# Kernel tuning notes

Measured on AMD Instinct MI355X. Metric: run time of the kernel, lower is better.

## Reference

```python
import jax, jax.numpy as jnp
import numpy as np
import math

D_MODEL = 128
N_HEAD = 8
D_K = D_MODEL // N_HEAD
NEG_INF = -1e30


def setup_inputs() -> dict:
    key = jax.random.key(0)
    ks = jax.random.split(key, 8)
    B, N, D = 4, 2048, D_MODEL
    s = 1.0 / math.sqrt(D)
    x = jax.random.normal(ks[0], (B, D, N), dtype=jnp.float32)
    mask = jnp.ones((B, N), dtype=jnp.float32)
    Wq = jax.random.normal(ks[1], (D, D), dtype=jnp.float32) * s
    Wk = jax.random.normal(ks[2], (D, D), dtype=jnp.float32) * s
    Wv = jax.random.normal(ks[3], (D, D), dtype=jnp.float32) * s
    Wfc = jax.random.normal(ks[4], (D, D), dtype=jnp.float32) * s
    z = jnp.zeros((D,), dtype=jnp.float32)
    return {"x": x, "mask": mask, "Wq": Wq, "bq": z, "Wk": Wk, "bk": z,
            "Wv": Wv, "bv": z, "Wfc": Wfc, "bfc": z}


def reference(x, mask, Wq, bq, Wk, bk, Wv, bv, Wfc, bfc):
    # x: [B, D, N], mask: [B, N]
    B, D, N = x.shape
    xt = jnp.swapaxes(x, 1, 2)  # [B, N, D]
    q = (xt @ Wq.T + bq).reshape(B, N, N_HEAD, D_K)
    k = (xt @ Wk.T + bk).reshape(B, N, N_HEAD, D_K)
    v = (xt @ Wv.T + bv).reshape(B, N, N_HEAD, D_K)
    # scores: [B, H, Nq, Nk]; NOTE: original scales by sqrt(d_model), not sqrt(d_k)
    scores = jnp.einsum('bnhd,bmhd->bhnm', q, k) / jnp.sqrt(jnp.float32(D))
    # multiplicative mask_logits over the key dimension
    m = mask[:, None, None, :]  # [B, 1, 1, Nk]
    scores = scores * m + (1.0 - m) * NEG_INF
    atten = jax.nn.softmax(scores, axis=-1)  # dropout is identity (p=0 / eval)
    out = jnp.einsum('bhnm,bmhd->bnhd', atten, v).reshape(B, N, D)
    out = out @ Wfc.T + bfc
    return jnp.swapaxes(out, 1, 2)  # [B, D, N]
```

## Files before the change

kernel.cpp:

```cpp
#include <hip/hip_runtime.h>
#include <stdint.h>

#define BSZ  4
#define NSEQ 2048
#define DM   128
#define NH   8
#define DK   16
#define LOG2E 1.4426950408889634f
#define SCALE_QL 0.1275156338341935f
#define M_FIX 18.0f

typedef __bf16          bf16x8v __attribute__((ext_vector_type(8)));
typedef float           f32x4   __attribute__((ext_vector_type(4)));
typedef float           f32x16  __attribute__((ext_vector_type(16)));
typedef unsigned short  u16x8   __attribute__((ext_vector_type(8)));
typedef unsigned short  u16x4   __attribute__((ext_vector_type(4)));
typedef unsigned int    u32x2   __attribute__((ext_vector_type(2)));
typedef unsigned int    u32x4   __attribute__((ext_vector_type(4)));

__device__ __forceinline__ unsigned short f2bf(float f) {
    unsigned u = __float_as_uint(f);
    u = (u + 0x7fffu + ((u >> 16) & 1u)) >> 16;
    return (unsigned short)u;
}

__device__ __forceinline__ unsigned int pack2bf(float a, float b) {
#if __has_builtin(__builtin_amdgcn_cvt_pk_bf16_f32)
    typedef __bf16 bf16x2 __attribute__((ext_vector_type(2)));
    bf16x2 v = __builtin_amdgcn_cvt_pk_bf16_f32(a, b);
    return __builtin_bit_cast(unsigned int, v);
#else
    return (unsigned)f2bf(a) | ((unsigned)f2bf(b) << 16);
#endif
}

__device__ __forceinline__ float exp2_(float x) {
#if __has_builtin(__builtin_amdgcn_exp2f)
    return __builtin_amdgcn_exp2f(x);
#else
    return exp2f(x);
#endif
}

__device__ __forceinline__ u16x8 cvt8(const float* p, float sc) {
    const f32x4 a = *reinterpret_cast<const f32x4*>(p);
    const f32x4 b = *reinterpret_cast<const f32x4*>(p + 4);
    u32x4 u = {pack2bf(a[0] * sc, a[1] * sc), pack2bf(a[2] * sc, a[3] * sc),
               pack2bf(b[0] * sc, b[1] * sc), pack2bf(b[2] * sc, b[3] * sc)};
    return __builtin_bit_cast(u16x8, u);
}

__device__ __forceinline__ f32x4 mfma16(u16x8 a, u16x8 b, f32x4 c) {
    return __builtin_amdgcn_mfma_f32_16x16x32_bf16(
        __builtin_bit_cast(bf16x8v, a), __builtin_bit_cast(bf16x8v, b), c, 0, 0, 0);
}
__device__ __forceinline__ f32x16 mfma32(u16x8 a, u16x8 b, f32x16 c) {
    return __builtin_amdgcn_mfma_f32_32x32x16_bf16(
        __builtin_bit_cast(bf16x8v, a), __builtin_bit_cast(bf16x8v, b), c, 0, 0, 0);
}

__global__ __launch_bounds__(192) void k_qkv(
    const float* __restrict__ x,
    const float* __restrict__ Wq, const float* __restrict__ bq,
    const float* __restrict__ Wk, const float* __restrict__ bk,
    const float* __restrict__ Wv, const float* __restrict__ bv,
    const float* __restrict__ Wfc, const float* __restrict__ mask,
    unsigned short* __restrict__ Q, unsigned short* __restrict__ Kb,
    unsigned short* __restrict__ Vt,
    unsigned short* __restrict__ WfcB, float* __restrict__ mbias)
{
    const int gt = blockIdx.x * 192 + threadIdx.x;
    if (gt < DM * DM) {
        WfcB[gt] = f2bf(Wfc[gt]);
    } else if (gt < DM * DM + BSZ * NSEQ) {
        const int i = gt - DM * DM;
        mbias[i] = (1.0f - mask[i]) * (-1e30f * LOG2E) - M_FIX;
    }

    const int lane = threadIdx.x & 63;
    const int mat  = threadIdx.x >> 6;
    const int c    = lane & 15;
    const int quad = lane >> 4;
    const int b    = blockIdx.x >> 8;
    const int n0   = ((blockIdx.x >> 1) & 127) << 4;
    const int th   = blockIdx.x & 1;

    u16x8 xf[4];
#pragma unroll
    for (int kk = 0; kk < 4; ++kk) {
        u16x8 u;
#pragma unroll
        for (int j = 0; j < 8; ++j)
            u[j] = f2bf(x[(b * DM + kk * 32 + quad * 8 + j) * NSEQ + n0 + c]);
        xf[kk] = u;
    }

    const float* W    = (mat == 0) ? Wq : (mat == 1) ? Wk : Wv;
    const float* bias = (mat == 0) ? bq : (mat == 1) ? bk : bv;
    const float  sc   = (mat == 0) ? SCALE_QL : 1.0f;

#pragma unroll
    for (int tt = 0; tt < 4; ++tt) {
        const int t = th * 4 + tt;
        f32x4 acc = {0.f, 0.f, 0.f, 0.f};
#pragma unroll
        for (int kk = 0; kk < 4; ++kk)
            acc = mfma16(cvt8(W + (t * 16 + c) * DM + kk * 32 + quad * 8, sc),
                         xf[kk], acc);
        if (mat == 2) {
#pragma unroll
            for (int r = 0; r < 4; ++r)
                Vt[((b * NH + t) * DK + quad * 4 + r) * NSEQ + n0 + c] =
                    f2bf(acc[r] + bias[t * 16 + quad * 4 + r]);
        } else {
            u16x4 pk;
#pragma unroll
            for (int r = 0; r < 4; ++r)
                pk[r] = f2bf(acc[r] + bias[t * 16 + quad * 4 + r] * sc);
            *reinterpret_cast<u16x4*>(
                (mat == 0 ? Q : Kb) + ((size_t)(b * NH + t) * NSEQ + n0 + c) * DK +
                quad * 4) = pk;
        }
    }
}

__global__ __launch_bounds__(256, 4) void k_attn(
    const unsigned short* __restrict__ Q,
    const unsigned short* __restrict__ Kb,
    const unsigned short* __restrict__ Vt,
    const float* __restrict__ mb2,
    unsigned short* __restrict__ AO)
{
    __shared__ __align__(16) char smem[17408];
    const int tid  = threadIdx.x;
    const int lane = tid & 63;
    const int w    = tid >> 6;
    const int q32  = lane & 31;
    const int hi   = lane >> 5;
    const int c    = lane & 15;
    const int quad = lane >> 4;

    const int b  = blockIdx.x >> 9;
    const int h  = (blockIdx.x >> 6) & 7;
    const int n0 = (blockIdx.x & 63) << 5;
    const int bh = b * NH + h;

    const u16x8 uq = *reinterpret_cast<const u16x8*>(
        Q + ((size_t)bh * NSEQ + n0 + q32) * DK + 8 * hi);

    const unsigned short* Kp = Kb + (size_t)bh * NSEQ * DK + 8 * hi;
    const unsigned short* Vp = Vt + ((size_t)bh * DK + c) * NSEQ + 8 * quad;
    const float*          mb = mb2 + b * NSEQ + 4 * hi;

    char* pbase = smem + w * 4352;
    char* wrow  = pbase + q32 * 136 + 8 * hi;
    const char* rrow0 = pbase + c * 136 + 16 * quad;
    const char* rrow1 = pbase + (c + 16) * 136 + 16 * quad;

    float l_acc = 0.f;
    f32x4 o0 = {0.f, 0.f, 0.f, 0.f}, o1 = {0.f, 0.f, 0.f, 0.f};
    const int kvb = w * (NSEQ / 4);

    for (int it = 0; it < 8; ++it) {
        const int kv0 = kvb + it * 64;
        f32x16 C0, C1;
#pragma unroll
        for (int g = 0; g < 4; ++g) {
            const f32x4 bg0 = *reinterpret_cast<const f32x4*>(mb + kv0 + 8 * g);
            const f32x4 bg1 = *reinterpret_cast<const f32x4*>(mb + kv0 + 32 + 8 * g);
#pragma unroll
            for (int r = 0; r < 4; ++r) {
                C0[4 * g + r] = bg0[r];
                C1[4 * g + r] = bg1[r];
            }
        }
        const u16x8 uk0 = *reinterpret_cast<const u16x8*>(Kp + (size_t)(kv0 + q32) * DK);
        const u16x8 uk1 = *reinterpret_cast<const u16x8*>(Kp + (size_t)(kv0 + 32 + q32) * DK);
        f32x16 S0 = mfma32(uk0, uq, C0);
        f32x16 S1 = mfma32(uk1, uq, C1);

#pragma unroll
        for (int i = 0; i < 16; ++i) {
            S0[i] = exp2_(S0[i]);
            S1[i] = exp2_(S1[i]);
        }
        float s16[16];
#pragma unroll
        for (int i = 0; i < 16; ++i) s16[i] = S0[i] + S1[i];
#pragma unroll
        for (int i = 0; i < 8; ++i) s16[i] += s16[i + 8];
#pragma unroll
        for (int i = 0; i < 4; ++i) s16[i] += s16[i + 4];
        l_acc += (s16[0] + s16[1]) + (s16[2] + s16[3]);

#pragma unroll
        for (int g = 0; g < 4; ++g) {
            u32x2 d0 = {pack2bf(S0[4 * g], S0[4 * g + 1]),
                        pack2bf(S0[4 * g + 2], S0[4 * g + 3])};
            u32x2 d1 = {pack2bf(S1[4 * g], S1[4 * g + 1]),
                        pack2bf(S1[4 * g + 2], S1[4 * g + 3])};
            *reinterpret_cast<u32x2*>(wrow + 16 * g) = d0;
            *reinterpret_cast<u32x2*>(wrow + 64 + 16 * g) = d1;
        }

#pragma unroll
        for (int t = 0; t < 2; ++t) {
            const u16x8 uv  = *reinterpret_cast<const u16x8*>(Vp + kv0 + 32 * t);
            const u16x8 up0 = *reinterpret_cast<const u16x8*>(rrow0 + 64 * t);
            const u16x8 up1 = *reinterpret_cast<const u16x8*>(rrow1 + 64 * t);
            o0 = mfma16(uv, up0, o0);
            o1 = mfma16(uv, up1, o1);
        }
    }

    l_acc += __shfl_xor(l_acc, 32, 64);

    __syncthreads();
    float* Lsm = reinterpret_cast<float*>(smem);
    float* Osm = reinterpret_cast<float*>(smem + 512);
    Lsm[w * 32 + q32] = l_acc;
    *reinterpret_cast<f32x4*>(Osm + w * 640 + c * 20 + 4 * quad)        = o0;
    *reinterpret_cast<f32x4*>(Osm + w * 640 + (c + 16) * 20 + 4 * quad) = o1;
    __syncthreads();

    const int q   = tid >> 3;
    const int dk2 = (tid & 7) * 2;
    const float l = Lsm[q] + Lsm[32 + q] + Lsm[64 + q] + Lsm[96 + q];
    const float* Oq = Osm + q * 20 + dk2;
    const float v0 = Oq[0] + Oq[640] + Oq[1280] + Oq[1920];
    const float v1 = Oq[1] + Oq[641] + Oq[1281] + Oq[1921];
    const float inv = 1.0f / l;
    *reinterpret_cast<unsigned int*>(
        AO + ((size_t)(b * NSEQ) + n0 + q) * DM + h * DK + dk2) =
        pack2bf(v0 * inv, v1 * inv);
}

__global__ __launch_bounds__(256) void k_fc(
    const unsigned short* __restrict__ AO,
    const unsigned short* __restrict__ WfcB, const float* __restrict__ bfc,
    float* __restrict__ out)
{
    const int lane = threadIdx.x & 63;
    const int w    = threadIdx.x >> 6;
    const int c    = lane & 15;
    const int quad = lane >> 4;
    const int b    = blockIdx.x >> 8;
    const int n0   = ((blockIdx.x >> 1) & 127) << 4;
    const int t    = (blockIdx.x & 1) * 4 + w;

    u16x8 af[4];
#pragma unroll
    for (int kk = 0; kk < 4; ++kk)
        af[kk] = *reinterpret_cast<const u16x8*>(
            AO + ((size_t)(b * NSEQ) + n0 + c) * DM + kk * 32 + quad * 8);

    f32x4 acc = {0.f, 0.f, 0.f, 0.f};
#pragma unroll
    for (int kk = 0; kk < 4; ++kk)
        acc = mfma16(*reinterpret_cast<const u16x8*>(
                         WfcB + (t * 16 + c) * DM + kk * 32 + quad * 8),
                     af[kk], acc);
#pragma unroll
    for (int r = 0; r < 4; ++r)
        out[(size_t)(b * DM + t * 16 + quad * 4 + r) * NSEQ + n0 + c] =
            acc[r] + bfc[t * 16 + quad * 4 + r];
}

extern "C" void kernel_launch(void* const* d_in, const int* in_sizes, int n_in,
                              void* d_out, int out_size, void* d_ws, size_t ws_size,
                              hipStream_t stream)
{
    const float* x    = (const float*)d_in[0];
    const float* mask = (const float*)d_in[1];
    const float* Wq   = (const float*)d_in[2];
    const float* bq   = (const float*)d_in[3];
    const float* Wk   = (const float*)d_in[4];
    const float* bk   = (const float*)d_in[5];
    const float* Wv   = (const float*)d_in[6];
    const float* bv   = (const float*)d_in[7];
    const float* Wfc  = (const float*)d_in[8];
    const float* bfc  = (const float*)d_in[9];
    float* out = (float*)d_out;

    const size_t QKV_ELEMS = (size_t)BSZ * NH * NSEQ * DK;
    unsigned short* Q    = (unsigned short*)d_ws;
    unsigned short* Kb   = Q + QKV_ELEMS;
    unsigned short* Vt   = Kb + QKV_ELEMS;
    unsigned short* AO   = Vt + QKV_ELEMS;
    unsigned short* WfcB = AO + QKV_ELEMS;
    float* mbias = (float*)(WfcB + DM * DM);

    k_qkv<<<1024, 192, 0, stream>>>(x, Wq, bq, Wk, bk, Wv, bv, Wfc, mask,
                                    Q, Kb, Vt, WfcB, mbias);
    k_attn<<<2048, 256, 0, stream>>>(Q, Kb, Vt, mbias, AO);
    k_fc<<<1024, 256, 0, stream>>>(AO, WfcB, bfc, out);
}
```

Before: 135.6 us.

## Stage x tile in LDS, double-buffer P, compute softmax denominators via MFMA

The QKV projection now uses 768-thread blocks that each load a 32-column x tile into shared memory once and share it across 12 waves, instead of every wave gathering x from global memory with strided loads. The attention kernel double-buffers the per-wave probability tile in LDS and unrolls the loop by two. It also replaces the scalar row-sum reduction with extra MFMAs against a ones vector. The goal is less redundant global traffic and fewer VALU adds. The cost is more LDS per block in the attention kernel, which may limit occupancy, plus extra MFMA work for the denominators.

New measurement: 132.4 us. 2.4% less time.

```diff
diff --git a/kernel.cpp b/kernel.cpp
--- a/kernel.cpp
+++ b/kernel.cpp
@@ -59,7 +59,7 @@
         __builtin_bit_cast(bf16x8v, a), __builtin_bit_cast(bf16x8v, b), c, 0, 0, 0);
 }
 
-__global__ __launch_bounds__(192) void k_qkv(
+__global__ __launch_bounds__(768) void k_qkv(
     const float* __restrict__ x,
     const float* __restrict__ Wq, const float* __restrict__ bq,
     const float* __restrict__ Wk, const float* __restrict__ bk,
@@ -69,7 +69,10 @@
     unsigned short* __restrict__ Vt,
     unsigned short* __restrict__ WfcB, float* __restrict__ mbias)
 {
-    const int gt = blockIdx.x * 192 + threadIdx.x;
+    __shared__ __align__(16) float xs[DM * 36];
+    const int tid = threadIdx.x;
+
+    const int gt = blockIdx.x * 768 + tid;
     if (gt < DM * DM) {
         WfcB[gt] = f2bf(Wfc[gt]);
     } else if (gt < DM * DM + BSZ * NSEQ) {
@@ -77,22 +80,36 @@
         mbias[i] = (1.0f - mask[i]) * (-1e30f * LOG2E) - M_FIX;
     }
 
-    const int lane = threadIdx.x & 63;
-    const int mat  = threadIdx.x >> 6;
+    const int b  = blockIdx.x >> 6;
+    const int n0 = (blockIdx.x & 63) << 5;
+
+#pragma unroll
+    for (int i = tid; i < 1024; i += 768) {
+        const int d = i >> 3, c4 = (i & 7) << 2;
+        *reinterpret_cast<f32x4*>(&xs[d * 36 + c4]) =
+            *reinterpret_cast<const f32x4*>(x + (size_t)(b * DM + d) * NSEQ + n0 + c4);
+    }
+    __syncthreads();
+
+    const int lane = tid & 63;
+    const int wv   = tid >> 6;
+    const int mat  = wv >> 2;
+    const int nt   = (wv >> 1) & 1;
+    const int th   = wv & 1;
     const int c    = lane & 15;
     const int quad = lane >> 4;
-    const int b    = blockIdx.x >> 8;
-    const int n0   = ((blockIdx.x >> 1) & 127) << 4;
-    const int th   = blockIdx.x & 1;
+    const int col  = n0 + nt * 16 + c;
 
     u16x8 xf[4];
 #pragma unroll
     for (int kk = 0; kk < 4; ++kk) {
-        u16x8 u;
+        float f[8];
 #pragma unroll
         for (int j = 0; j < 8; ++j)
-            u[j] = f2bf(x[(b * DM + kk * 32 + quad * 8 + j) * NSEQ + n0 + c]);
-        xf[kk] = u;
+            f[j] = xs[(kk * 32 + quad * 8 + j) * 36 + nt * 16 + c];
+        u32x4 u = {pack2bf(f[0], f[1]), pack2bf(f[2], f[3]),
+                   pack2bf(f[4], f[5]), pack2bf(f[6], f[7])};
+        xf[kk] = __builtin_bit_cast(u16x8, u);
     }
 
     const float* W    = (mat == 0) ? Wq : (mat == 1) ? Wk : Wv;
@@ -110,7 +127,7 @@
         if (mat == 2) {
 #pragma unroll
             for (int r = 0; r < 4; ++r)
-                Vt[((b * NH + t) * DK + quad * 4 + r) * NSEQ + n0 + c] =
+                Vt[((b * NH + t) * DK + quad * 4 + r) * NSEQ + col] =
                     f2bf(acc[r] + bias[t * 16 + quad * 4 + r]);
         } else {
             u16x4 pk;
@@ -118,7 +135,7 @@
             for (int r = 0; r < 4; ++r)
                 pk[r] = f2bf(acc[r] + bias[t * 16 + quad * 4 + r] * sc);
             *reinterpret_cast<u16x4*>(
-                (mat == 0 ? Q : Kb) + ((size_t)(b * NH + t) * NSEQ + n0 + c) * DK +
+                (mat == 0 ? Q : Kb) + ((size_t)(b * NH + t) * NSEQ + col) * DK +
                 quad * 4) = pk;
         }
     }
@@ -131,7 +148,7 @@
     const float* __restrict__ mb2,
     unsigned short* __restrict__ AO)
 {
-    __shared__ __align__(16) char smem[17408];
+    __shared__ __align__(16) char smem[34816];
     const int tid  = threadIdx.x;
     const int lane = tid & 63;
     const int w    = tid >> 6;
@@ -152,17 +169,24 @@
     const unsigned short* Vp = Vt + ((size_t)bh * DK + c) * NSEQ + 8 * quad;
     const float*          mb = mb2 + b * NSEQ + 4 * hi;
 
-    char* pbase = smem + w * 4352;
-    char* wrow  = pbase + q32 * 136 + 8 * hi;
-    const char* rrow0 = pbase + c * 136 + 16 * quad;
-    const char* rrow1 = pbase + (c + 16) * 136 + 16 * quad;
-
-    float l_acc = 0.f;
+    u16x8 uone;
+#pragma unroll
+    for (int j = 0; j < 8; ++j) uone[j] = 0x3F80;
+
+    char* pb = smem + w * 8704;
+
     f32x4 o0 = {0.f, 0.f, 0.f, 0.f}, o1 = {0.f, 0.f, 0.f, 0.f};
+    f32x4 l0 = {0.f, 0.f, 0.f, 0.f}, l1 = {0.f, 0.f, 0.f, 0.f};
     const int kvb = w * (NSEQ / 4);
 
+#pragma unroll 2
     for (int it = 0; it < 8; ++it) {
         const int kv0 = kvb + it * 64;
+        char* pbase = pb + (it & 1) * 4352;
+        char* wrow  = pbase + q32 * 136 + 8 * hi;
+        const char* rrow0 = pbase + c * 136 + 16 * quad;
+        const char* rrow1 = pbase + (c + 16) * 136 + 16 * quad;
+
         f32x16 C0, C1;
 #pragma unroll
         for (int g = 0; g < 4; ++g) {
@@ -184,14 +208,6 @@
             S0[i] = exp2_(S0[i]);
             S1[i] = exp2_(S1[i]);
         }
-        float s16[16];
-#pragma unroll
-        for (int i = 0; i < 16; ++i) s16[i] = S0[i] + S1[i];
-#pragma unroll
-        for (int i = 0; i < 8; ++i) s16[i] += s16[i + 8];
-#pragma unroll
-        for (int i = 0; i < 4; ++i) s16[i] += s16[i + 4];
-        l_acc += (s16[0] + s16[1]) + (s16[2] + s16[3]);
 
 #pragma unroll
         for (int g = 0; g < 4; ++g) {
@@ -210,15 +226,16 @@
             const u16x8 up1 = *reinterpret_cast<const u16x8*>(rrow1 + 64 * t);
             o0 = mfma16(uv, up0, o0);
             o1 = mfma16(uv, up1, o1);
-        }
-    }
-
-    l_acc += __shfl_xor(l_acc, 32, 64);
+            l0 = mfma16(uone, up0, l0);
+            l1 = mfma16(uone, up1, l1);
+        }
+    }
 
     __syncthreads();
     float* Lsm = reinterpret_cast<float*>(smem);
     float* Osm = reinterpret_cast<float*>(smem + 512);
-    Lsm[w * 32 + q32] = l_acc;
+    Lsm[w * 32 + c]      = l0[0];
+    Lsm[w * 32 + 16 + c] = l1[0];
     *reinterpret_cast<f32x4*>(Osm + w * 640 + c * 20 + 4 * quad)        = o0;
     *reinterpret_cast<f32x4*>(Osm + w * 640 + (c + 16) * 20 + 4 * quad) = o1;
     __syncthreads();
@@ -290,8 +307,8 @@
     unsigned short* WfcB = AO + QKV_ELEMS;
     float* mbias = (float*)(WfcB + DM * DM);
 
-    k_qkv<<<1024, 192, 0, stream>>>(x, Wq, bq, Wk, bk, Wv, bv, Wfc, mask,
-                                    Q, Kb, Vt, WfcB, mbias);
+    k_qkv<<<256, 768, 0, stream>>>(x, Wq, bq, Wk, bk, Wv, bv, Wfc, mask,
+                                   Q, Kb, Vt, WfcB, mbias);
     k_attn<<<2048, 256, 0, stream>>>(Q, Kb, Vt, mbias, AO);
     k_fc<<<1024, 256, 0, stream>>>(AO, WfcB, bfc, out);
 }
```
